# Performance work log

Measured on AMD Instinct MI355X. Metric: run time of the kernel, lower is better.

## Reference

```python
import jax, jax.numpy as jnp
import numpy as np

NUM_TASKS = 200_000
NUM_DATA = 100_000
E_DT = 1_000_000
E_TT = 1_000_000
N_DEV = 8
TASK_D, DATA_D, DEV_D, H = 12, 5, 12, 64


def _leaky(x):
    return jnp.where(x > 0, x, 0.01 * x)


def _layernorm(x, g, b, eps=1e-5):
    m = jnp.mean(x, axis=-1, keepdims=True)
    v = jnp.mean((x - m) ** 2, axis=-1, keepdims=True)
    return (x - m) * jax.lax.rsqrt(v + eps) * g + b


def _edge_conv(x, src, dst, W1, b1, W2, b2, n_nodes):
    # PyG EdgeConv: message = mlp(cat[x_i, x_j - x_i]), aggregated (add) at target i = dst
    xi = x[dst]                    # [E, d]
    xj = x[src]                    # [E, d]
    h = jnp.concatenate([xi, xj - xi], axis=-1)   # [E, 2d]
    h = _leaky(h @ W1 + b1)
    h = h @ W2 + b2
    return jax.ops.segment_sum(h, dst, num_segments=n_nodes)


def setup_inputs() -> dict:
    key = jax.random.key(0)
    ks = jax.random.split(key, 24)
    s = 0.05
    inp = {
        'data_x': jax.random.normal(ks[0], (NUM_DATA, DATA_D), jnp.float32),
        'tasks_x': jax.random.normal(ks[1], (NUM_TASKS, TASK_D), jnp.float32),
        'devices_x': jax.random.normal(ks[2], (N_DEV, DEV_D), jnp.float32),
        'time_x': jax.random.uniform(ks[3], (1, 1), jnp.float32) * 100000.0,
        'dt_src': jax.random.randint(ks[4], (E_DT,), 0, NUM_DATA, jnp.int32),
        'dt_dst': jax.random.randint(ks[5], (E_DT,), 0, NUM_TASKS, jnp.int32),
        'tt_src': jax.random.randint(ks[6], (E_TT,), 0, NUM_TASKS, jnp.int32),
        'tt_dst': jax.random.randint(ks[7], (E_TT,), 0, NUM_TASKS, jnp.int32),
        'counts': jax.random.randint(ks[8], (1,), 1, NUM_TASKS, jnp.int32),
        # GraphConv (bipartite): lin_rel on aggregated src msgs (with bias), lin_root on dst (no bias)
        'gc_W_rel': jax.random.normal(ks[9], (DATA_D, H), jnp.float32) * s,
        'gc_b_rel': jnp.zeros((H,), jnp.float32),
        'gc_W_root': jax.random.normal(ks[10], (TASK_D, H), jnp.float32) * s,
        'gc_ln_g': jnp.ones((H,), jnp.float32),
        'gc_ln_b': jnp.zeros((H,), jnp.float32),
        # EdgeConv dependants (edges as-is)
        'dep_W1': jax.random.normal(ks[11], (2 * H, H), jnp.float32) * s,
        'dep_b1': jnp.zeros((H,), jnp.float32),
        'dep_W2': jax.random.normal(ks[12], (H, H), jnp.float32) * s,
        'dep_b2': jnp.zeros((H,), jnp.float32),
        'dep_ln_g': jnp.ones((H,), jnp.float32),
        'dep_ln_b': jnp.zeros((H,), jnp.float32),
        # EdgeConv dependencies (edges flipped)
        'rev_W1': jax.random.normal(ks[13], (2 * H, H), jnp.float32) * s,
        'rev_b1': jnp.zeros((H,), jnp.float32),
        'rev_W2': jax.random.normal(ks[14], (H, H), jnp.float32) * s,
        'rev_b2': jnp.zeros((H,), jnp.float32),
        'rev_ln_g': jnp.ones((H,), jnp.float32),
        'rev_ln_b': jnp.zeros((H,), jnp.float32),
        # device layer: Linear(n_dev*dev_dim + 1 -> H)
        'dev_W': jax.random.normal(ks[15], (N_DEV * DEV_D + 1, H), jnp.float32) * s,
        'dev_b': jnp.zeros((H,), jnp.float32),
        # project down: Linear(2H -> H)
        'proj_W': jax.random.normal(ks[16], (2 * H, H), jnp.float32) * s,
        'proj_b': jnp.zeros((H,), jnp.float32),
    }
    return inp


def reference(data_x, tasks_x, devices_x, time_x, dt_src, dt_dst, tt_src, tt_dst, counts,
              gc_W_rel, gc_b_rel, gc_W_root, gc_ln_g, gc_ln_b,
              dep_W1, dep_b1, dep_W2, dep_b2, dep_ln_g, dep_ln_b,
              rev_W1, rev_b1, rev_W2, rev_b2, rev_ln_g, rev_ln_b,
              dev_W, dev_b, proj_W, proj_b):
    n_tasks = tasks_x.shape[0]
    # DataTaskGraphConv: scatter-add data features into tasks, then linear + root linear
    agg = jax.ops.segment_sum(data_x[dt_src], dt_dst, num_segments=n_tasks)  # [N_t, DATA_D]
    fused = agg @ gc_W_rel + gc_b_rel + tasks_x @ gc_W_root                  # [N_t, H]
    fused = _leaky(_layernorm(fused, gc_ln_g, gc_ln_b))
    # TaskTaskEdgeConv dependants (forward edges) and dependencies (flipped edges)
    dep = _edge_conv(fused, tt_src, tt_dst, dep_W1, dep_b1, dep_W2, dep_b2, n_tasks)
    dep = _leaky(_layernorm(dep, dep_ln_g, dep_ln_b))
    rev = _edge_conv(fused, tt_dst, tt_src, rev_W1, rev_b1, rev_W2, rev_b2, n_tasks)
    rev = _leaky(_layernorm(rev, rev_ln_g, rev_ln_b))
    # device branch
    dev = devices_x.reshape(-1)                      # [N_DEV*DEV_D]
    t = jax.lax.stop_gradient(time_x / 100000.0)[0]  # [1]
    dev = jnp.concatenate([dev, t], axis=-1)
    dev = _leaky(dev @ dev_W + dev_b)                # [H]
    # task fusion
    tf = jnp.concatenate([dep, rev], axis=-1)        # [N_t, 2H]
    tf = _leaky(tf @ proj_W + proj_b)                # [N_t, H]
    candidate = tf[0]                                # [H]
    c0 = jnp.maximum(counts[0], 1).astype(tf.dtype)
    global_state = jnp.sum(tf, axis=0) / c0          # [H]
    return jnp.concatenate([global_state, candidate, dev], axis=-1)  # [3H]
```

## Files before the change

### kernel.cpp

```cpp
#include <hip/hip_runtime.h>

#define DEVFN static __device__ __forceinline__

typedef __attribute__((ext_vector_type(8))) short short8;
typedef __attribute__((ext_vector_type(4))) float f32x4;

#define NB_SCAN 256
#define NB3 64
#define BUCKET 120
#define MAXBUK 2048

DEVFN float leaky(float x) { return x > 0.f ? x : 0.01f * x; }

DEVFN float wsum(float v) {
#pragma unroll
    for (int o = 32; o > 0; o >>= 1) v += __shfl_xor(v, o, 64);
    return v;
}

DEVFN unsigned short f2bf(float f) {
    unsigned u = __float_as_uint(f);
    unsigned r = (u + 0x7FFFu + ((u >> 16) & 1u)) >> 16;
    return (unsigned short)r;
}
DEVFN float bf2f(unsigned short h) { return __uint_as_float(((unsigned)h) << 16); }

__global__ void k_bhist(const int* __restrict__ tt_src, const int* __restrict__ tt_dst,
                        const int* __restrict__ dt_dst,
                        int* __restrict__ cnt_d, int* __restrict__ cnt_s, int* __restrict__ cnt_t,
                        int n_tt, int n_dt, int nbuk) {
    __shared__ int h[2 * MAXBUK];
    int blk = blockIdx.x, y = blockIdx.y;
    for (int k = threadIdx.x; k < nbuk; k += 256) {
        h[k] = 0;
        if (y == 0) h[MAXBUK + k] = 0;
    }
    __syncthreads();
    int n = (y == 0) ? n_tt : n_dt;
    int chunk = (n + NB3 - 1) / NB3;
    int e0 = blk * chunk;
    int e1 = e0 + chunk < n ? e0 + chunk : n;
    if (y == 0) {
        for (int i = e0 + threadIdx.x; i < e1; i += 256) {
            unsigned d = (unsigned)tt_dst[i], s = (unsigned)tt_src[i];
            atomicAdd(&h[d / BUCKET], 1);
            atomicAdd(&h[MAXBUK + s / BUCKET], 1);
        }
    } else {
        for (int i = e0 + threadIdx.x; i < e1; i += 256) {
            unsigned d = (unsigned)dt_dst[i];
            atomicAdd(&h[d / BUCKET], 1);
        }
    }
    __syncthreads();
    for (int k = threadIdx.x; k < nbuk; k += 256) {
        if (y == 0) {
            cnt_d[k * NB3 + blk] = h[k];
            cnt_s[k * NB3 + blk] = h[MAXBUK + k];
        } else {
            cnt_t[k * NB3 + blk] = h[k];
        }
    }
}

__global__ void k_scanA(const int* __restrict__ d0, const int* __restrict__ d1,
                        const int* __restrict__ d2, int* __restrict__ bsum, int n) {
    const int* deg = blockIdx.y == 0 ? d0 : (blockIdx.y == 1 ? d1 : d2);
    int chunk = (n + NB_SCAN - 1) / NB_SCAN;
    int base = blockIdx.x * chunk;
    int end = base + chunk;
    if (end > n) end = n;
    int s = 0;
    for (int i = base + threadIdx.x; i < end; i += 256) s += deg[i];
    int lane = threadIdx.x & 63, wid = threadIdx.x >> 6;
#pragma unroll
    for (int o = 32; o > 0; o >>= 1) s += __shfl_xor(s, o, 64);
    __shared__ int w[4];
    if (lane == 0) w[wid] = s;
    __syncthreads();
    if (threadIdx.x == 0) bsum[blockIdx.y * NB_SCAN + blockIdx.x] = w[0] + w[1] + w[2] + w[3];
}

__global__ void k_scanC(const int* __restrict__ d0, const int* __restrict__ d1,
                        const int* __restrict__ d2, const int* __restrict__ bsum,
                        int* __restrict__ o0, int* __restrict__ o1, int* __restrict__ o2,
                        int n) {
    const int* deg = blockIdx.y == 0 ? d0 : (blockIdx.y == 1 ? d1 : d2);
    int* off = blockIdx.y == 0 ? o0 : (blockIdx.y == 1 ? o1 : o2);
    __shared__ int bl[NB_SCAN];
    int t = threadIdx.x;
    int bv = bsum[blockIdx.y * NB_SCAN + t];
    bl[t] = bv;
    __syncthreads();
    for (int o = 1; o < NB_SCAN; o <<= 1) {
        int u = (t >= o) ? bl[t - o] : 0;
        __syncthreads();
        bl[t] += u;
        __syncthreads();
    }
    int blockpref = (blockIdx.x > 0) ? bl[blockIdx.x - 1] : 0;
    __syncthreads();

    int chunk = (n + NB_SCAN - 1) / NB_SCAN;
    int base = blockIdx.x * chunk;
    int end = base + chunk;
    if (end > n) end = n;
    int sub = (chunk + 255) >> 8;
    int s0 = base + t * sub;
    int s1 = s0 + sub;
    if (s0 > end) s0 = end;
    if (s1 > end) s1 = end;
    int s = 0;
    for (int i = s0; i < s1; ++i) s += deg[i];
    __shared__ int lds[256];
    lds[t] = s;
    __syncthreads();
    for (int o = 1; o < 256; o <<= 1) {
        int u = (t >= o) ? lds[t - o] : 0;
        __syncthreads();
        lds[t] += u;
        __syncthreads();
    }
    int ex = blockpref + lds[t] - s;
    for (int i = s0; i < s1; ++i) {
        off[i] = ex;
        ex += deg[i];
    }
}

__global__ void k_bdump(const int* __restrict__ tt_src, const int* __restrict__ tt_dst,
                        const int* __restrict__ dt_src, const int* __restrict__ dt_dst,
                        const int* __restrict__ base_d, const int* __restrict__ base_s,
                        const int* __restrict__ base_t,
                        unsigned* __restrict__ packed_d, unsigned* __restrict__ packed_s,
                        unsigned* __restrict__ packed_t,
                        int n_tt, int n_dt, int nbuk) {
    __shared__ int cur[2 * MAXBUK];
    int blk = blockIdx.x, y = blockIdx.y;
    for (int k = threadIdx.x; k < nbuk; k += 256) {
        if (y == 0) {
            cur[k] = base_d[k * NB3 + blk];
            cur[MAXBUK + k] = base_s[k * NB3 + blk];
        } else {
            cur[k] = base_t[k * NB3 + blk];
        }
    }
    __syncthreads();
    int n = (y == 0) ? n_tt : n_dt;
    int chunk = (n + NB3 - 1) / NB3;
    int e0 = blk * chunk;
    int e1 = e0 + chunk < n ? e0 + chunk : n;
    if (y == 0) {
        for (int i = e0 + threadIdx.x; i < e1; i += 256) {
            unsigned s = (unsigned)tt_src[i], d = (unsigned)tt_dst[i];
            unsigned bd = d / BUCKET, bs = s / BUCKET;
            int pd = atomicAdd(&cur[bd], 1);
            packed_d[pd] = ((d - bd * BUCKET) << 22) | s;
            int ps = atomicAdd(&cur[MAXBUK + bs], 1);
            packed_s[ps] = ((s - bs * BUCKET) << 22) | d;
        }
    } else {
        for (int i = e0 + threadIdx.x; i < e1; i += 256) {
            unsigned s = (unsigned)dt_src[i], d = (unsigned)dt_dst[i];
            unsigned bd = d / BUCKET;
            int pt = atomicAdd(&cur[bd], 1);
            packed_t[pt] = ((d - bd * BUCKET) << 22) | s;
        }
    }
}

__global__ void __launch_bounds__(256) k_bcsr(
    const unsigned* __restrict__ packed_d, const unsigned* __restrict__ packed_s,
    const int* __restrict__ base_d, const int* __restrict__ base_s,
    unsigned* __restrict__ other_d, unsigned* __restrict__ other_s,
    int* __restrict__ off_d, int* __restrict__ off_s,
    int* __restrict__ deg_d, int* __restrict__ deg_s,
    int n_tt, int n_tasks, int nbuk) {
    int y = blockIdx.y;
    const unsigned* packed = y ? packed_s : packed_d;
    const int* bases = y ? base_s : base_d;
    unsigned* other = y ? other_s : other_d;
    int* offo = y ? off_s : off_d;
    int* dego = y ? deg_s : deg_d;
    __shared__ int cnt[128];
    __shared__ int sc[128];
    __shared__ int cur[128];
    int tid = threadIdx.x;
    int b = blockIdx.x;
    int r0 = b * BUCKET;
    int rcount = n_tasks - r0 < BUCKET ? n_tasks - r0 : BUCKET;
    int a0 = bases[b * NB3];
    int a1 = (b + 1 < nbuk) ? bases[(b + 1) * NB3] : n_tt;
    if (tid < 128) cnt[tid] = 0;
    __syncthreads();
    for (int e = a0 + tid; e < a1; e += 256) atomicAdd(&cnt[packed[e] >> 22], 1);
    __syncthreads();
    if (tid < 128) sc[tid] = cnt[tid];
    __syncthreads();
    for (int o = 1; o < 128; o <<= 1) {
        int v = (tid >= o && tid < 128) ? sc[tid - o] : 0;
        __syncthreads();
        if (tid < 128) sc[tid] += v;
        __syncthreads();
    }
    if (tid < 128) {
        int ex = sc[tid] - cnt[tid];
        cur[tid] = ex;
        if (tid < rcount) {
            offo[r0 + tid] = a0 + ex;
            dego[r0 + tid] = cnt[tid];
        }
    }
    if (b == nbuk - 1 && tid == 0) offo[n_tasks] = n_tt;
    __syncthreads();
    for (int e = a0 + tid; e < a1; e += 256) {
        unsigned p = packed[e];
        int dl = p >> 22;
        int pos = atomicAdd(&cur[dl], 1);
        other[(size_t)a0 + pos] = p & 0x3FFFFF;
    }
}

__global__ void k_bagg(const float* __restrict__ data_x, const unsigned* __restrict__ packed_t,
                       const int* __restrict__ base_t, float* __restrict__ agg,
                       int n_dt, int n_tasks, int nbuk) {
    __shared__ float aggL[BUCKET * 5];
    int b = blockIdx.x;
    int r0 = b * BUCKET;
    int rcount = n_tasks - r0 < BUCKET ? n_tasks - r0 : BUCKET;
    for (int k = threadIdx.x; k < BUCKET * 5; k += 256) aggL[k] = 0.f;
    __syncthreads();
    int a0 = base_t[b * NB3];
    int a1 = (b + 1 < nbuk) ? base_t[(b + 1) * NB3] : n_dt;
    for (int e = a0 + threadIdx.x; e < a1; e += 256) {
        unsigned p = packed_t[e];
        int s = p & 0x3FFFFF;
        int dl = p >> 22;
        const float* xp = data_x + (size_t)s * 5;
#pragma unroll
        for (int c = 0; c < 5; ++c) atomicAdd(&aggL[dl * 5 + c], xp[c]);
    }
    __syncthreads();
    for (int k = threadIdx.x; k < rcount * 5; k += 256) agg[(size_t)r0 * 5 + k] = aggL[k];
}

__global__ void k_fused(const float* __restrict__ agg, const float* __restrict__ tasks_x,
                        const float* __restrict__ Wrel, const float* __restrict__ brel,
                        const float* __restrict__ Wroot,
                        const float* __restrict__ g, const float* __restrict__ b,
                        unsigned short* __restrict__ xh, int n_rows) {
    int lane = threadIdx.x & 63;
    int wave = (blockIdx.x * blockDim.x + threadIdx.x) >> 6;
    int nwaves = (gridDim.x * blockDim.x) >> 6;
    float wrel[5], wroot[12];
#pragma unroll
    for (int k = 0; k < 5; ++k) wrel[k] = Wrel[k * 64 + lane];
#pragma unroll
    for (int k = 0; k < 12; ++k) wroot[k] = Wroot[k * 64 + lane];
    float bj = brel[lane], gj = g[lane], bbj = b[lane];
    for (int r = wave; r < n_rows; r += nwaves) {
        float f = bj;
#pragma unroll
        for (int k = 0; k < 5; ++k) f = fmaf(agg[(size_t)r * 5 + k], wrel[k], f);
#pragma unroll
        for (int k = 0; k < 12; ++k) f = fmaf(tasks_x[(size_t)r * 12 + k], wroot[k], f);
        float m = wsum(f) * 0.015625f;
        float d = f - m;
        float v = wsum(d * d) * 0.015625f;
        float y = fmaf(d * rsqrtf(v + 1e-5f), gj, bbj);
        xh[(size_t)r * 64 + lane] = f2bf(leaky(y));
    }
}

__global__ void k_prepw(const float* __restrict__ W1d, const float* __restrict__ W2d,
                        const float* __restrict__ W1r, const float* __restrict__ W2r,
                        const float* __restrict__ PW, unsigned short* __restrict__ wf) {
    int lane = threadIdx.x;
    int r16 = lane & 15, g = lane >> 4;
    for (int c = 0; c < 2; ++c) {
        const float* W1 = c ? W1r : W1d;
        const float* W2 = c ? W2r : W2d;
        unsigned short* out = wf + (size_t)c * 48 * 512;
        for (int kk = 0; kk < 2; ++kk)
            for (int nt = 0; nt < 4; ++nt)
                for (int j = 0; j < 8; ++j) {
                    int k = kk * 32 + g * 8 + j, col = nt * 16 + r16;
                    int fr = (kk * 4 + nt) * 2;
                    float vc = W1[k * 64 + col] - W1[(64 + k) * 64 + col];
                    unsigned short hi = f2bf(vc);
                    out[(size_t)fr * 512 + lane * 8 + j] = hi;
                    out[(size_t)(fr + 1) * 512 + lane * 8 + j] = f2bf(vc - bf2f(hi));
                    float vt = W1[(64 + k) * 64 + col];
                    hi = f2bf(vt);
                    out[(size_t)(16 + fr) * 512 + lane * 8 + j] = hi;
                    out[(size_t)(16 + fr + 1) * 512 + lane * 8 + j] = f2bf(vt - bf2f(hi));
                    float v2 = W2[k * 64 + col];
                    hi = f2bf(v2);
                    out[(size_t)(32 + fr) * 512 + lane * 8 + j] = hi;
                    out[(size_t)(32 + fr + 1) * 512 + lane * 8 + j] = f2bf(v2 - bf2f(hi));
                }
    }
    unsigned short* out = wf + (size_t)96 * 512;
    for (int kk = 0; kk < 4; ++kk)
        for (int nt = 0; nt < 4; ++nt)
            for (int j = 0; j < 8; ++j) {
                int k = kk * 32 + g * 8 + j, col = nt * 16 + r16;
                int fr = (kk * 4 + nt) * 2;
                float v = PW[k * 64 + col];
                unsigned short hi = f2bf(v);
                out[(size_t)fr * 512 + lane * 8 + j] = hi;
                out[(size_t)(fr + 1) * 512 + lane * 8 + j] = f2bf(v - bf2f(hi));
            }
}

__global__ void __launch_bounds__(256, 2) k_ct(
    const unsigned short* __restrict__ xh, const unsigned short* __restrict__ wfall,
    const float* __restrict__ b1d, const float* __restrict__ b1r,
    unsigned short* __restrict__ Hd, unsigned short* __restrict__ Hr,
    unsigned short* __restrict__ Tbd, unsigned short* __restrict__ Tbr,
    int n_rows, int n_tiles) {
    int y = blockIdx.y;
    const unsigned short* wf = wfall + (size_t)y * 48 * 512;
    const float* b1 = y ? b1r : b1d;
    unsigned short* Cb = y ? Hr : Hd;
    unsigned short* Tb = y ? Tbr : Tbd;
    int lane = threadIdx.x & 63;
    int r16 = lane & 15, g = lane >> 4;
    int wave = (blockIdx.x * blockDim.x + threadIdx.x) >> 6;
    int nwaves = (gridDim.x * blockDim.x) >> 6;
    short8 cw[2][4][2], tw[2][4][2];
#pragma unroll
    for (int kk = 0; kk < 2; ++kk)
#pragma unroll
        for (int nt = 0; nt < 4; ++nt)
#pragma unroll
            for (int hl = 0; hl < 2; ++hl) {
                int fr = (kk * 4 + nt) * 2 + hl;
                cw[kk][nt][hl] = *(const short8*)(wf + (size_t)fr * 512 + lane * 8);
                tw[kk][nt][hl] = *(const short8*)(wf + (size_t)(16 + fr) * 512 + lane * 8);
            }
    float b1v[4];
#pragma unroll
    for (int nt = 0; nt < 4; ++nt) b1v[nt] = b1[nt * 16 + r16];
    for (int t = wave; t < n_tiles; t += nwaves) {
        int r0 = t * 16;
        int ra = r0 + r16;
        ra = ra < n_rows ? ra : n_rows - 1;
        short8 af[2];
        af[0] = *(const short8*)(xh + (size_t)ra * 64 + g * 8);
        af[1] = *(const short8*)(xh + (size_t)ra * 64 + 32 + g * 8);
        f32x4 accC[4], accT[4];
#pragma unroll
        for (int nt = 0; nt < 4; ++nt) {
            accC[nt] = (f32x4){b1v[nt], b1v[nt], b1v[nt], b1v[nt]};
            accT[nt] = (f32x4){0.f, 0.f, 0.f, 0.f};
        }
#pragma unroll
        for (int kk = 0; kk < 2; ++kk)
#pragma unroll
            for (int nt = 0; nt < 4; ++nt) {
                accC[nt] = __builtin_amdgcn_mfma_f32_16x16x32_bf16(af[kk], cw[kk][nt][0], accC[nt], 0, 0, 0);
                accC[nt] = __builtin_amdgcn_mfma_f32_16x16x32_bf16(af[kk], cw[kk][nt][1], accC[nt], 0, 0, 0);
                accT[nt] = __builtin_amdgcn_mfma_f32_16x16x32_bf16(af[kk], tw[kk][nt][0], accT[nt], 0, 0, 0);
                accT[nt] = __builtin_amdgcn_mfma_f32_16x16x32_bf16(af[kk], tw[kk][nt][1], accT[nt], 0, 0, 0);
            }
#pragma unroll
        for (int nt = 0; nt < 4; ++nt)
#pragma unroll
            for (int q = 0; q < 4; ++q) {
                int row = r0 + g * 4 + q;
                if (row < n_rows) {
                    Cb[(size_t)row * 64 + nt * 16 + r16] = f2bf(accC[nt][q]);
                    Tb[(size_t)row * 64 + nt * 16 + r16] = f2bf(accT[nt][q]);
                }
            }
    }
}

__global__ void k_edge(unsigned short* __restrict__ Hd, unsigned short* __restrict__ Hr,
                       const unsigned short* __restrict__ Tbd, const unsigned short* __restrict__ Tbr,
                       const int* __restrict__ off_d, const int* __restrict__ off_s,
                       const unsigned* __restrict__ other_d, const unsigned* __restrict__ other_s,
                       int n_tasks) {
    int lane = threadIdx.x & 63;
    int wave = (blockIdx.x * blockDim.x + threadIdx.x) >> 6;
    int nwaves = (gridDim.x * blockDim.x) >> 6;
    for (int i = wave; i < n_tasks; i += nwaves) {
        int pd = off_d[i], d1 = off_d[i + 1];
        int ps = off_s[i], s1 = off_s[i + 1];
        float cvd = bf2f(Hd[(size_t)i * 64 + lane]);
        float cvr = bf2f(Hr[(size_t)i * 64 + lane]);
        float accd = 0.f, accr = 0.f;
        while (pd + 2 <= d1 && ps + 2 <= s1) {
            unsigned jd0 = other_d[pd], jd1 = other_d[pd + 1];
            unsigned js0 = other_s[ps], js1 = other_s[ps + 1];
            float td0 = bf2f(Tbd[(size_t)jd0 * 64 + lane]);
            float td1 = bf2f(Tbd[(size_t)jd1 * 64 + lane]);
            float tr0 = bf2f(Tbr[(size_t)js0 * 64 + lane]);
            float tr1 = bf2f(Tbr[(size_t)js1 * 64 + lane]);
            accd += leaky(cvd + td0);
            accd += leaky(cvd + td1);
            accr += leaky(cvr + tr0);
            accr += leaky(cvr + tr1);
            pd += 2;
            ps += 2;
        }
        for (; pd + 4 <= d1; pd += 4) {
            float t0 = bf2f(Tbd[(size_t)other_d[pd] * 64 + lane]);
            float t1 = bf2f(Tbd[(size_t)other_d[pd + 1] * 64 + lane]);
            float t2 = bf2f(Tbd[(size_t)other_d[pd + 2] * 64 + lane]);
            float t3 = bf2f(Tbd[(size_t)other_d[pd + 3] * 64 + lane]);
            accd += leaky(cvd + t0);
            accd += leaky(cvd + t1);
            accd += leaky(cvd + t2);
            accd += leaky(cvd + t3);
        }
        for (; pd < d1; ++pd) accd += leaky(cvd + bf2f(Tbd[(size_t)other_d[pd] * 64 + lane]));
        for (; ps + 4 <= s1; ps += 4) {
            float t0 = bf2f(Tbr[(size_t)other_s[ps] * 64 + lane]);
            float t1 = bf2f(Tbr[(size_t)other_s[ps + 1] * 64 + lane]);
            float t2 = bf2f(Tbr[(size_t)other_s[ps + 2] * 64 + lane]);
            float t3 = bf2f(Tbr[(size_t)other_s[ps + 3] * 64 + lane]);
            accr += leaky(cvr + t0);
            accr += leaky(cvr + t1);
            accr += leaky(cvr + t2);
            accr += leaky(cvr + t3);
        }
        for (; ps < s1; ++ps) accr += leaky(cvr + bf2f(Tbr[(size_t)other_s[ps] * 64 + lane]));
        Hd[(size_t)i * 64 + lane] = f2bf(accd);
        Hr[(size_t)i * 64 + lane] = f2bf(accr);
    }
}

__global__ void __launch_bounds__(256, 2) k_post(
    unsigned short* __restrict__ Hd, unsigned short* __restrict__ Hr,
    const unsigned short* __restrict__ wfall,
    const float* __restrict__ b2d, const float* __restrict__ b2r,
    const int* __restrict__ deg_d, const int* __restrict__ deg_s,
    int n_rows, int n_tiles) {
    int y = blockIdx.y;
    unsigned short* H = y ? Hr : Hd;
    const unsigned short* wf = wfall + (size_t)(y ? 48 + 32 : 32) * 512;
    const float* b2 = y ? b2r : b2d;
    const int* deg = y ? deg_s : deg_d;
    int lane = threadIdx.x & 63;
    int r16 = lane & 15, g = lane >> 4;
    int wave = (blockIdx.x * blockDim.x + threadIdx.x) >> 6;
    int nwaves = (gridDim.x * blockDim.x) >> 6;
    short8 w2[2][4][2];
#pragma unroll
    for (int kk = 0; kk < 2; ++kk)
#pragma unroll
        for (int nt = 0; nt < 4; ++nt)
#pragma unroll
            for (int hl = 0; hl < 2; ++hl)
                w2[kk][nt][hl] =
                    *(const short8*)(wf + (size_t)((kk * 4 + nt) * 2 + hl) * 512 + lane * 8);
    float b2v[4];
#pragma unroll
    for (int nt = 0; nt < 4; ++nt) b2v[nt] = b2[nt * 16 + r16];
    for (int t = wave; t < n_tiles; t += nwaves) {
        int r0 = t * 16;
        int ra = r0 + r16;
        ra = ra < n_rows ? ra : n_rows - 1;
        short8 af[2];
        af[0] = *(const short8*)(H + (size_t)ra * 64 + g * 8);
        af[1] = *(const short8*)(H + (size_t)ra * 64 + 32 + g * 8);
        float degf[4];
#pragma unroll
        for (int q = 0; q < 4; ++q) {
            int r = r0 + g * 4 + q;
            r = r < n_rows ? r : n_rows - 1;
            degf[q] = (float)deg[r];
        }
        f32x4 acc[4];
#pragma unroll
        for (int nt = 0; nt < 4; ++nt)
#pragma unroll
            for (int q = 0; q < 4; ++q) acc[nt][q] = degf[q] * b2v[nt];
#pragma unroll
        for (int kk = 0; kk < 2; ++kk)
#pragma unroll
            for (int nt = 0; nt < 4; ++nt) {
                acc[nt] = __builtin_amdgcn_mfma_f32_16x16x32_bf16(af[kk], w2[kk][nt][0], acc[nt], 0, 0, 0);
                acc[nt] = __builtin_amdgcn_mfma_f32_16x16x32_bf16(af[kk], w2[kk][nt][1], acc[nt], 0, 0, 0);
            }
#pragma unroll
        for (int nt = 0; nt < 4; ++nt)
#pragma unroll
            for (int q = 0; q < 4; ++q) {
                int row = r0 + g * 4 + q;
                if (row < n_rows) H[(size_t)row * 64 + nt * 16 + r16] = f2bf(acc[nt][q]);
            }
    }
}

__global__ void __launch_bounds__(256, 2) k_finalize(
    const unsigned short* __restrict__ dep_raw, const unsigned short* __restrict__ rev_raw,
    const float* __restrict__ dg, const float* __restrict__ db,
    const float* __restrict__ rg, const float* __restrict__ rb,
    const unsigned short* __restrict__ pwf, const float* __restrict__ pb,
    float* __restrict__ out, float* __restrict__ gsum, int n_rows, int n_tiles) {
    __shared__ float red[4][64];
    int lane = threadIdx.x & 63;
    int wid = threadIdx.x >> 6;
    int r16 = lane & 15, g = lane >> 4;
    int wave = (blockIdx.x * blockDim.x + threadIdx.x) >> 6;
    int nwaves = (gridDim.x * blockDim.x) >> 6;

    short8 wf[4][4][2];
#pragma unroll
    for (int kk = 0; kk < 4; ++kk)
#pragma unroll
        for (int nt = 0; nt < 4; ++nt)
#pragma unroll
            for (int hl = 0; hl < 2; ++hl)
                wf[kk][nt][hl] =
                    *(const short8*)(pwf + (size_t)((kk * 4 + nt) * 2 + hl) * 512 + lane * 8);

    f32x4 gd0 = *(const f32x4*)(dg + g * 8), gd1 = *(const f32x4*)(dg + g * 8 + 4);
    f32x4 gd2 = *(const f32x4*)(dg + 32 + g * 8), gd3 = *(const f32x4*)(dg + 32 + g * 8 + 4);
    f32x4 bd0 = *(const f32x4*)(db + g * 8), bd1 = *(const f32x4*)(db + g * 8 + 4);
    f32x4 bd2 = *(const f32x4*)(db + 32 + g * 8), bd3 = *(const f32x4*)(db + 32 + g * 8 + 4);
    f32x4 gr0 = *(const f32x4*)(rg + g * 8), gr1 = *(const f32x4*)(rg + g * 8 + 4);
    f32x4 gr2 = *(const f32x4*)(rg + 32 + g * 8), gr3 = *(const f32x4*)(rg + 32 + g * 8 + 4);
    f32x4 br0 = *(const f32x4*)(rb + g * 8), br1 = *(const f32x4*)(rb + g * 8 + 4);
    f32x4 br2 = *(const f32x4*)(rb + 32 + g * 8), br3 = *(const f32x4*)(rb + 32 + g * 8 + 4);

    float b2v[4];
#pragma unroll
    for (int nt = 0; nt < 4; ++nt) b2v[nt] = pb[nt * 16 + r16];
    float gacc[4] = {0.f, 0.f, 0.f, 0.f};

    for (int t = wave; t < n_tiles; t += nwaves) {
        int r0 = t * 16;
        int ra = r0 + r16;
        ra = ra < n_rows ? ra : n_rows - 1;
        const unsigned short* dp = dep_raw + (size_t)ra * 64;
        const unsigned short* rp = rev_raw + (size_t)ra * 64;
        short8 hd0 = *(const short8*)(dp + g * 8);
        short8 hd1 = *(const short8*)(dp + 32 + g * 8);
        short8 hr0 = *(const short8*)(rp + g * 8);
        short8 hr1 = *(const short8*)(rp + 32 + g * 8);
        f32x4 xd0, xd1, xd2, xd3, xr0, xr1, xr2, xr3;
#pragma unroll
        for (int j = 0; j < 4; ++j) {
            xd0[j] = bf2f((unsigned short)hd0[j]);
            xd1[j] = bf2f((unsigned short)hd0[4 + j]);
            xd2[j] = bf2f((unsigned short)hd1[j]);
            xd3[j] = bf2f((unsigned short)hd1[4 + j]);
            xr0[j] = bf2f((unsigned short)hr0[j]);
            xr1[j] = bf2f((unsigned short)hr0[4 + j]);
            xr2[j] = bf2f((unsigned short)hr1[j]);
            xr3[j] = bf2f((unsigned short)hr1[4 + j]);
        }

        float sd = 0.f, qd = 0.f, sr = 0.f, qr = 0.f;
#pragma unroll
        for (int j = 0; j < 4; ++j) {
            sd += xd0[j] + xd1[j] + xd2[j] + xd3[j];
            qd = fmaf(xd0[j], xd0[j], qd); qd = fmaf(xd1[j], xd1[j], qd);
            qd = fmaf(xd2[j], xd2[j], qd); qd = fmaf(xd3[j], xd3[j], qd);
            sr += xr0[j] + xr1[j] + xr2[j] + xr3[j];
            qr = fmaf(xr0[j], xr0[j], qr); qr = fmaf(xr1[j], xr1[j], qr);
            qr = fmaf(xr2[j], xr2[j], qr); qr = fmaf(xr3[j], xr3[j], qr);
        }
#pragma unroll
        for (int o = 16; o <= 32; o <<= 1) {
            sd += __shfl_xor(sd, o, 64); qd += __shfl_xor(qd, o, 64);
            sr += __shfl_xor(sr, o, 64); qr += __shfl_xor(qr, o, 64);
        }
        float md = sd * 0.015625f;
        float rstd_d = rsqrtf(fmaf(qd, 0.015625f, -md * md) + 1e-5f);
        float mr = sr * 0.015625f;
        float rstd_r = rsqrtf(fmaf(qr, 0.015625f, -mr * mr) + 1e-5f);

        short8 af[4];
#pragma unroll
        for (int j = 0; j < 4; ++j) {
            af[0][j]     = (short)f2bf(leaky(fmaf((xd0[j] - md) * rstd_d, gd0[j], bd0[j])));
            af[0][4 + j] = (short)f2bf(leaky(fmaf((xd1[j] - md) * rstd_d, gd1[j], bd1[j])));
            af[1][j]     = (short)f2bf(leaky(fmaf((xd2[j] - md) * rstd_d, gd2[j], bd2[j])));
            af[1][4 + j] = (short)f2bf(leaky(fmaf((xd3[j] - md) * rstd_d, gd3[j], bd3[j])));
            af[2][j]     = (short)f2bf(leaky(fmaf((xr0[j] - mr) * rstd_r, gr0[j], br0[j])));
            af[2][4 + j] = (short)f2bf(leaky(fmaf((xr1[j] - mr) * rstd_r, gr1[j], br1[j])));
            af[3][j]     = (short)f2bf(leaky(fmaf((xr2[j] - mr) * rstd_r, gr2[j], br2[j])));
            af[3][4 + j] = (short)f2bf(leaky(fmaf((xr3[j] - mr) * rstd_r, gr3[j], br3[j])));
        }

        f32x4 acc[4];
#pragma unroll
        for (int nt = 0; nt < 4; ++nt) acc[nt] = (f32x4){b2v[nt], b2v[nt], b2v[nt], b2v[nt]};
#pragma unroll
        for (int kk = 0; kk < 4; ++kk)
#pragma unroll
            for (int nt = 0; nt < 4; ++nt) {
                acc[nt] = __builtin_amdgcn_mfma_f32_16x16x32_bf16(af[kk], wf[kk][nt][0], acc[nt], 0, 0, 0);
                acc[nt] = __builtin_amdgcn_mfma_f32_16x16x32_bf16(af[kk], wf[kk][nt][1], acc[nt], 0, 0, 0);
            }
#pragma unroll
        for (int nt = 0; nt < 4; ++nt)
#pragma unroll
            for (int q = 0; q < 4; ++q) {
                float tf = leaky(acc[nt][q]);
                int grow = r0 + g * 4 + q;
                if (grow < n_rows) gacc[nt] += tf;
                if (grow == 0) out[64 + nt * 16 + r16] = tf;
            }
    }
#pragma unroll
    for (int nt = 0; nt < 4; ++nt) {
        gacc[nt] += __shfl_xor(gacc[nt], 16, 64);
        gacc[nt] += __shfl_xor(gacc[nt], 32, 64);
    }
    if (g == 0) {
#pragma unroll
        for (int nt = 0; nt < 4; ++nt) red[wid][nt * 16 + r16] = gacc[nt];
    }
    __syncthreads();
    if (threadIdx.x < 64) {
        float ssum = red[0][threadIdx.x] + red[1][threadIdx.x] +
                     red[2][threadIdx.x] + red[3][threadIdx.x];
        atomicAdd(&gsum[threadIdx.x], ssum);
    }
}

__global__ void k_tail(const float* __restrict__ gsum, const int* __restrict__ counts,
                       const float* __restrict__ devx, const float* __restrict__ timex,
                       const float* __restrict__ dW, const float* __restrict__ dB,
                       float* __restrict__ out) {
    int j = threadIdx.x;
    if (j >= 64) return;
    int c = counts[0];
    if (c < 1) c = 1;
    out[j] = gsum[j] / (float)c;
    float t = timex[0] * 1e-5f;
    float acc = dB[j];
    for (int k = 0; k < 96; ++k) acc = fmaf(devx[k], dW[k * 64 + j], acc);
    acc = fmaf(t, dW[96 * 64 + j], acc);
    out[128 + j] = leaky(acc);
}

extern "C" void kernel_launch(void* const* d_in, const int* in_sizes, int n_in,
                              void* d_out, int out_size, void* d_ws, size_t ws_size,
                              hipStream_t stream) {
    const float* data_x    = (const float*)d_in[0];
    const float* tasks_x   = (const float*)d_in[1];
    const float* devices_x = (const float*)d_in[2];
    const float* time_x    = (const float*)d_in[3];
    const int*   dt_src    = (const int*)d_in[4];
    const int*   dt_dst    = (const int*)d_in[5];
    const int*   tt_src    = (const int*)d_in[6];
    const int*   tt_dst    = (const int*)d_in[7];
    const int*   counts    = (const int*)d_in[8];
    const float* gc_W_rel  = (const float*)d_in[9];
    const float* gc_b_rel  = (const float*)d_in[10];
    const float* gc_W_root = (const float*)d_in[11];
    const float* gc_ln_g   = (const float*)d_in[12];
    const float* gc_ln_b   = (const float*)d_in[13];
    const float* dep_W1    = (const float*)d_in[14];
    const float* dep_b1    = (const float*)d_in[15];
    const float* dep_W2    = (const float*)d_in[16];
    const float* dep_b2    = (const float*)d_in[17];
    const float* dep_ln_g  = (const float*)d_in[18];
    const float* dep_ln_b  = (const float*)d_in[19];
    const float* rev_W1    = (const float*)d_in[20];
    const float* rev_b1    = (const float*)d_in[21];
    const float* rev_W2    = (const float*)d_in[22];
    const float* rev_b2    = (const float*)d_in[23];
    const float* rev_ln_g  = (const float*)d_in[24];
    const float* rev_ln_b  = (const float*)d_in[25];
    const float* dev_W     = (const float*)d_in[26];
    const float* dev_b     = (const float*)d_in[27];
    const float* proj_W    = (const float*)d_in[28];
    const float* proj_b    = (const float*)d_in[29];

    int n_tasks = in_sizes[1] / 12;
    int n_dt = in_sizes[4];
    int n_tt = in_sizes[6];
    int n_tiles = (n_tasks + 15) / 16;
    int nbuk = (n_tasks + BUCKET - 1) / BUCKET;
    int nscan = nbuk * NB3;

    char* ws = (char*)d_ws;
    size_t off = 0;
    auto alloc = [&](size_t bytes) {
        char* p = ws + off;
        off += (bytes + 255) & ~(size_t)255;
        return p;
    };
    float* agg            = (float*)alloc((size_t)n_tasks * 5 * 4);
    unsigned short* xh    = (unsigned short*)alloc((size_t)n_tasks * 64 * 2);
    unsigned short* Hd    = (unsigned short*)alloc((size_t)n_tasks * 64 * 2);
    unsigned short* Hr    = (unsigned short*)alloc((size_t)n_tasks * 64 * 2);
    unsigned short* Tbd   = (unsigned short*)alloc((size_t)n_tasks * 64 * 2);
    unsigned short* Tbr   = (unsigned short*)alloc((size_t)n_tasks * 64 * 2);
    int* cnt_d            = (int*)alloc((size_t)nscan * 4);
    int* cnt_s            = (int*)alloc((size_t)nscan * 4);
    int* cnt_t            = (int*)alloc((size_t)nscan * 4);
    int* base_d           = (int*)alloc((size_t)nscan * 4);
    int* base_s           = (int*)alloc((size_t)nscan * 4);
    int* base_t           = (int*)alloc((size_t)nscan * 4);
    unsigned* packed_d    = (unsigned*)alloc((size_t)n_tt * 4);
    unsigned* packed_s    = (unsigned*)alloc((size_t)n_tt * 4);
    unsigned* packed_t    = (unsigned*)alloc((size_t)n_dt * 4);
    unsigned* other_d     = (unsigned*)alloc((size_t)n_tt * 4);
    unsigned* other_s     = (unsigned*)alloc((size_t)n_tt * 4);
    int* off_d            = (int*)alloc(((size_t)n_tasks + 1) * 4);
    int* off_s            = (int*)alloc(((size_t)n_tasks + 1) * 4);
    int* deg_d            = (int*)alloc((size_t)n_tasks * 4);
    int* deg_s            = (int*)alloc((size_t)n_tasks * 4);
    int* bsum             = (int*)alloc(3 * NB_SCAN * 4);
    float* gsum           = (float*)alloc(64 * 4);
    unsigned short* wfrag = (unsigned short*)alloc((size_t)128 * 512 * 2);

    hipMemsetAsync(gsum, 0, 64 * 4, stream);

    k_prepw<<<1, 64, 0, stream>>>(dep_W1, dep_W2, rev_W1, rev_W2, proj_W, wfrag);

    k_bhist<<<dim3(NB3, 2), 256, 0, stream>>>(tt_src, tt_dst, dt_dst,
                                              cnt_d, cnt_s, cnt_t, n_tt, n_dt, nbuk);
    k_scanA<<<dim3(NB_SCAN, 3), 256, 0, stream>>>(cnt_d, cnt_s, cnt_t, bsum, nscan);
    k_scanC<<<dim3(NB_SCAN, 3), 256, 0, stream>>>(cnt_d, cnt_s, cnt_t, bsum,
                                                  base_d, base_s, base_t, nscan);
    k_bdump<<<dim3(NB3, 2), 256, 0, stream>>>(tt_src, tt_dst, dt_src, dt_dst,
                                              base_d, base_s, base_t,
                                              packed_d, packed_s, packed_t, n_tt, n_dt, nbuk);
    k_bcsr<<<dim3(nbuk, 2), 256, 0, stream>>>(packed_d, packed_s, base_d, base_s,
                                              other_d, other_s, off_d, off_s,
                                              deg_d, deg_s, n_tt, n_tasks, nbuk);

    k_bagg<<<nbuk, 256, 0, stream>>>(data_x, packed_t, base_t, agg, n_dt, n_tasks, nbuk);
    k_fused<<<2048, 256, 0, stream>>>(agg, tasks_x, gc_W_rel, gc_b_rel, gc_W_root,
                                      gc_ln_g, gc_ln_b, xh, n_tasks);

    k_ct<<<dim3(2048, 2), 256, 0, stream>>>(xh, wfrag, dep_b1, rev_b1, Hd, Hr, Tbd, Tbr,
                                            n_tasks, n_tiles);
    k_edge<<<4096, 256, 0, stream>>>(Hd, Hr, Tbd, Tbr, off_d, off_s,
                                     other_d, other_s, n_tasks);
    k_post<<<dim3(2048, 2), 256, 0, stream>>>(Hd, Hr, wfrag, dep_b2, rev_b2,
                                              deg_d, deg_s, n_tasks, n_tiles);

    k_finalize<<<2048, 256, 0, stream>>>(Hd, Hr, dep_ln_g, dep_ln_b,
                                         rev_ln_g, rev_ln_b, wfrag + (size_t)96 * 512, proj_b,
                                         (float*)d_out, gsum, n_tasks, n_tiles);
    k_tail<<<1, 64, 0, stream>>>(gsum, counts, devices_x, time_x, dev_W, dev_b, (float*)d_out);
}
```

Baseline: 431.2 us.

## Fuse post-aggregation W2 GEMM, layernorm and projection into one kernel

```diff
diff --git a/kernel.cpp b/kernel.cpp
--- a/kernel.cpp
+++ b/kernel.cpp
@@ -277,40 +277,47 @@
                         const float* __restrict__ PW, unsigned short* __restrict__ wf) {
     int lane = threadIdx.x;
     int r16 = lane & 15, g = lane >> 4;
-    for (int c = 0; c < 2; ++c) {
+    int b = blockIdx.x;
+    if (b < 16) {
+        int c = b >> 3;
+        int tup = b & 7;
+        int kk = tup >> 2, nt = tup & 3;
         const float* W1 = c ? W1r : W1d;
         const float* W2 = c ? W2r : W2d;
         unsigned short* out = wf + (size_t)c * 48 * 512;
-        for (int kk = 0; kk < 2; ++kk)
-            for (int nt = 0; nt < 4; ++nt)
-                for (int j = 0; j < 8; ++j) {
-                    int k = kk * 32 + g * 8 + j, col = nt * 16 + r16;
-                    int fr = (kk * 4 + nt) * 2;
-                    float vc = W1[k * 64 + col] - W1[(64 + k) * 64 + col];
-                    unsigned short hi = f2bf(vc);
-                    out[(size_t)fr * 512 + lane * 8 + j] = hi;
-                    out[(size_t)(fr + 1) * 512 + lane * 8 + j] = f2bf(vc - bf2f(hi));
-                    float vt = W1[(64 + k) * 64 + col];
-                    hi = f2bf(vt);
-                    out[(size_t)(16 + fr) * 512 + lane * 8 + j] = hi;
-                    out[(size_t)(16 + fr + 1) * 512 + lane * 8 + j] = f2bf(vt - bf2f(hi));
-                    float v2 = W2[k * 64 + col];
-                    hi = f2bf(v2);
-                    out[(size_t)(32 + fr) * 512 + lane * 8 + j] = hi;
-                    out[(size_t)(32 + fr + 1) * 512 + lane * 8 + j] = f2bf(v2 - bf2f(hi));
-                }
-    }
-    unsigned short* out = wf + (size_t)96 * 512;
-    for (int kk = 0; kk < 4; ++kk)
-        for (int nt = 0; nt < 4; ++nt)
+        int fr = (kk * 4 + nt) * 2;
+#pragma unroll
+        for (int j = 0; j < 8; ++j) {
+            int k = kk * 32 + g * 8 + j, col = nt * 16 + r16;
+            float vc = W1[k * 64 + col] - W1[(64 + k) * 64 + col];
+            unsigned short hi = f2bf(vc);
+            out[(size_t)fr * 512 + lane * 8 + j] = hi;
+            out[(size_t)(fr + 1) * 512 + lane * 8 + j] = f2bf(vc - bf2f(hi));
+            float vt = W1[(64 + k) * 64 + col];
+            hi = f2bf(vt);
+            out[(size_t)(16 + fr) * 512 + lane * 8 + j] = hi;
+            out[(size_t)(16 + fr + 1) * 512 + lane * 8 + j] = f2bf(vt - bf2f(hi));
+            float v2 = W2[k * 64 + col];
+            hi = f2bf(v2);
+            out[(size_t)(32 + fr) * 512 + lane * 8 + j] = hi;
+            out[(size_t)(32 + fr + 1) * 512 + lane * 8 + j] = f2bf(v2 - bf2f(hi));
+        }
+    } else {
+        unsigned short* out = wf + (size_t)96 * 512;
+        int t0 = (b - 16) * 4;
+        for (int tt = t0; tt < t0 + 4; ++tt) {
+            int kk = tt >> 2, nt = tt & 3;
+            int fr = (kk * 4 + nt) * 2;
+#pragma unroll
             for (int j = 0; j < 8; ++j) {
                 int k = kk * 32 + g * 8 + j, col = nt * 16 + r16;
-                int fr = (kk * 4 + nt) * 2;
                 float v = PW[k * 64 + col];
                 unsigned short hi = f2bf(v);
                 out[(size_t)fr * 512 + lane * 8 + j] = hi;
                 out[(size_t)(fr + 1) * 512 + lane * 8 + j] = f2bf(v - bf2f(hi));
             }
+        }
+    }
 }
 
 __global__ void __launch_bounds__(256, 2) k_ct(
@@ -432,181 +439,167 @@
     }
 }
 
-__global__ void __launch_bounds__(256, 2) k_post(
-    unsigned short* __restrict__ Hd, unsigned short* __restrict__ Hr,
+__global__ void __launch_bounds__(256, 2) k_pf(
+    const unsigned short* __restrict__ Hd, const unsigned short* __restrict__ Hr,
     const unsigned short* __restrict__ wfall,
     const float* __restrict__ b2d, const float* __restrict__ b2r,
     const int* __restrict__ deg_d, const int* __restrict__ deg_s,
-    int n_rows, int n_tiles) {
-    int y = blockIdx.y;
-    unsigned short* H = y ? Hr : Hd;
-    const unsigned short* wf = wfall + (size_t)(y ? 48 + 32 : 32) * 512;
-    const float* b2 = y ? b2r : b2d;
-    const int* deg = y ? deg_s : deg_d;
-    int lane = threadIdx.x & 63;
-    int r16 = lane & 15, g = lane >> 4;
-    int wave = (blockIdx.x * blockDim.x + threadIdx.x) >> 6;
-    int nwaves = (gridDim.x * blockDim.x) >> 6;
-    short8 w2[2][4][2];
-#pragma unroll
-    for (int kk = 0; kk < 2; ++kk)
-#pragma unroll
-        for (int nt = 0; nt < 4; ++nt)
-#pragma unroll
-            for (int hl = 0; hl < 2; ++hl)
-                w2[kk][nt][hl] =
-                    *(const short8*)(wf + (size_t)((kk * 4 + nt) * 2 + hl) * 512 + lane * 8);
-    float b2v[4];
-#pragma unroll
-    for (int nt = 0; nt < 4; ++nt) b2v[nt] = b2[nt * 16 + r16];
-    for (int t = wave; t < n_tiles; t += nwaves) {
-        int r0 = t * 16;
-        int ra = r0 + r16;
-        ra = ra < n_rows ? ra : n_rows - 1;
-        short8 af[2];
-        af[0] = *(const short8*)(H + (size_t)ra * 64 + g * 8);
-        af[1] = *(const short8*)(H + (size_t)ra * 64 + 32 + g * 8);
-        float degf[4];
-#pragma unroll
-        for (int q = 0; q < 4; ++q) {
-            int r = r0 + g * 4 + q;
-            r = r < n_rows ? r : n_rows - 1;
-            degf[q] = (float)deg[r];
-        }
-        f32x4 acc[4];
-#pragma unroll
-        for (int nt = 0; nt < 4; ++nt)
-#pragma unroll
-            for (int q = 0; q < 4; ++q) acc[nt][q] = degf[q] * b2v[nt];
-#pragma unroll
-        for (int kk = 0; kk < 2; ++kk)
-#pragma unroll
-            for (int nt = 0; nt < 4; ++nt) {
-                acc[nt] = __builtin_amdgcn_mfma_f32_16x16x32_bf16(af[kk], w2[kk][nt][0], acc[nt], 0, 0, 0);
-                acc[nt] = __builtin_amdgcn_mfma_f32_16x16x32_bf16(af[kk], w2[kk][nt][1], acc[nt], 0, 0, 0);
-            }
-#pragma unroll
-        for (int nt = 0; nt < 4; ++nt)
-#pragma unroll
-            for (int q = 0; q < 4; ++q) {
-                int row = r0 + g * 4 + q;
-                if (row < n_rows) H[(size_t)row * 64 + nt * 16 + r16] = f2bf(acc[nt][q]);
-            }
-    }
-}
-
-__global__ void __launch_bounds__(256, 2) k_finalize(
-    const unsigned short* __restrict__ dep_raw, const unsigned short* __restrict__ rev_raw,
     const float* __restrict__ dg, const float* __restrict__ db,
     const float* __restrict__ rg, const float* __restrict__ rb,
-    const unsigned short* __restrict__ pwf, const float* __restrict__ pb,
+    const float* __restrict__ pb,
     float* __restrict__ out, float* __restrict__ gsum, int n_rows, int n_tiles) {
+    __shared__ unsigned short ldsT[4][16][136];
     __shared__ float red[4][64];
     int lane = threadIdx.x & 63;
-    int wid = threadIdx.x >> 6;
+    int w = threadIdx.x >> 6;
     int r16 = lane & 15, g = lane >> 4;
-    int wave = (blockIdx.x * blockDim.x + threadIdx.x) >> 6;
-    int nwaves = (gridDim.x * blockDim.x) >> 6;
-
-    short8 wf[4][4][2];
-#pragma unroll
-    for (int kk = 0; kk < 4; ++kk)
-#pragma unroll
-        for (int nt = 0; nt < 4; ++nt)
-#pragma unroll
-            for (int hl = 0; hl < 2; ++hl)
-                wf[kk][nt][hl] =
-                    *(const short8*)(pwf + (size_t)((kk * 4 + nt) * 2 + hl) * 512 + lane * 8);
-
-    f32x4 gd0 = *(const f32x4*)(dg + g * 8), gd1 = *(const f32x4*)(dg + g * 8 + 4);
-    f32x4 gd2 = *(const f32x4*)(dg + 32 + g * 8), gd3 = *(const f32x4*)(dg + 32 + g * 8 + 4);
-    f32x4 bd0 = *(const f32x4*)(db + g * 8), bd1 = *(const f32x4*)(db + g * 8 + 4);
-    f32x4 bd2 = *(const f32x4*)(db + 32 + g * 8), bd3 = *(const f32x4*)(db + 32 + g * 8 + 4);
-    f32x4 gr0 = *(const f32x4*)(rg + g * 8), gr1 = *(const f32x4*)(rg + g * 8 + 4);
-    f32x4 gr2 = *(const f32x4*)(rg + 32 + g * 8), gr3 = *(const f32x4*)(rg + 32 + g * 8 + 4);
-    f32x4 br0 = *(const f32x4*)(rb + g * 8), br1 = *(const f32x4*)(rb + g * 8 + 4);
-    f32x4 br2 = *(const f32x4*)(rb + 32 + g * 8), br3 = *(const f32x4*)(rb + 32 + g * 8 + 4);
-
-    float b2v[4];
-#pragma unroll
-    for (int nt = 0; nt < 4; ++nt) b2v[nt] = pb[nt * 16 + r16];
+
+    float gdv[4], bdv[4], grv[4], brv[4], b2dv[4], b2rv[4], pbv[4];
+#pragma unroll
+    for (int nt = 0; nt < 4; ++nt) {
+        int c = nt * 16 + r16;
+        gdv[nt] = dg[c]; bdv[nt] = db[c];
+        grv[nt] = rg[c]; brv[nt] = rb[c];
+        b2dv[nt] = b2d[c]; b2rv[nt] = b2r[c];
+        pbv[nt] = pb[c];
+    }
     float gacc[4] = {0.f, 0.f, 0.f, 0.f};
 
-    for (int t = wave; t < n_tiles; t += nwaves) {
-        int r0 = t * 16;
-        int ra = r0 + r16;
+    for (int t = blockIdx.x; t < n_tiles; t += gridDim.x) {
+        int R0 = t * 64 + w * 16;
+        int ra = R0 + r16;
         ra = ra < n_rows ? ra : n_rows - 1;
-        const unsigned short* dp = dep_raw + (size_t)ra * 64;
-        const unsigned short* rp = rev_raw + (size_t)ra * 64;
-        short8 hd0 = *(const short8*)(dp + g * 8);
-        short8 hd1 = *(const short8*)(dp + 32 + g * 8);
-        short8 hr0 = *(const short8*)(rp + g * 8);
-        short8 hr1 = *(const short8*)(rp + 32 + g * 8);
-        f32x4 xd0, xd1, xd2, xd3, xr0, xr1, xr2, xr3;
-#pragma unroll
-        for (int j = 0; j < 4; ++j) {
-            xd0[j] = bf2f((unsigned short)hd0[j]);
-            xd1[j] = bf2f((unsigned short)hd0[4 + j]);
-            xd2[j] = bf2f((unsigned short)hd1[j]);
-            xd3[j] = bf2f((unsigned short)hd1[4 + j]);
-            xr0[j] = bf2f((unsigned short)hr0[j]);
-            xr1[j] = bf2f((unsigned short)hr0[4 + j]);
-            xr2[j] = bf2f((unsigned short)hr1[j]);
-            xr3[j] = bf2f((unsigned short)hr1[4 + j]);
-        }
-
-        float sd = 0.f, qd = 0.f, sr = 0.f, qr = 0.f;
-#pragma unroll
-        for (int j = 0; j < 4; ++j) {
-            sd += xd0[j] + xd1[j] + xd2[j] + xd3[j];
-            qd = fmaf(xd0[j], xd0[j], qd); qd = fmaf(xd1[j], xd1[j], qd);
-            qd = fmaf(xd2[j], xd2[j], qd); qd = fmaf(xd3[j], xd3[j], qd);
-            sr += xr0[j] + xr1[j] + xr2[j] + xr3[j];
-            qr = fmaf(xr0[j], xr0[j], qr); qr = fmaf(xr1[j], xr1[j], qr);
-            qr = fmaf(xr2[j], xr2[j], qr); qr = fmaf(xr3[j], xr3[j], qr);
-        }
-#pragma unroll
-        for (int o = 16; o <= 32; o <<= 1) {
-            sd += __shfl_xor(sd, o, 64); qd += __shfl_xor(qd, o, 64);
-            sr += __shfl_xor(sr, o, 64); qr += __shfl_xor(qr, o, 64);
-        }
-        float md = sd * 0.015625f;
-        float rstd_d = rsqrtf(fmaf(qd, 0.015625f, -md * md) + 1e-5f);
-        float mr = sr * 0.015625f;
-        float rstd_r = rsqrtf(fmaf(qr, 0.015625f, -mr * mr) + 1e-5f);
-
-        short8 af[4];
-#pragma unroll
-        for (int j = 0; j < 4; ++j) {
-            af[0][j]     = (short)f2bf(leaky(fmaf((xd0[j] - md) * rstd_d, gd0[j], bd0[j])));
-            af[0][4 + j] = (short)f2bf(leaky(fmaf((xd1[j] - md) * rstd_d, gd1[j], bd1[j])));
-            af[1][j]     = (short)f2bf(leaky(fmaf((xd2[j] - md) * rstd_d, gd2[j], bd2[j])));
-            af[1][4 + j] = (short)f2bf(leaky(fmaf((xd3[j] - md) * rstd_d, gd3[j], bd3[j])));
-            af[2][j]     = (short)f2bf(leaky(fmaf((xr0[j] - mr) * rstd_r, gr0[j], br0[j])));
-            af[2][4 + j] = (short)f2bf(leaky(fmaf((xr1[j] - mr) * rstd_r, gr1[j], br1[j])));
-            af[3][j]     = (short)f2bf(leaky(fmaf((xr2[j] - mr) * rstd_r, gr2[j], br2[j])));
-            af[3][4 + j] = (short)f2bf(leaky(fmaf((xr3[j] - mr) * rstd_r, gr3[j], br3[j])));
-        }
-
-        f32x4 acc[4];
-#pragma unroll
-        for (int nt = 0; nt < 4; ++nt) acc[nt] = (f32x4){b2v[nt], b2v[nt], b2v[nt], b2v[nt]};
-#pragma unroll
-        for (int kk = 0; kk < 4; ++kk)
-#pragma unroll
-            for (int nt = 0; nt < 4; ++nt) {
-                acc[nt] = __builtin_amdgcn_mfma_f32_16x16x32_bf16(af[kk], wf[kk][nt][0], acc[nt], 0, 0, 0);
-                acc[nt] = __builtin_amdgcn_mfma_f32_16x16x32_bf16(af[kk], wf[kk][nt][1], acc[nt], 0, 0, 0);
-            }
-#pragma unroll
-        for (int nt = 0; nt < 4; ++nt)
+        {
+            short8 af[2];
+            af[0] = *(const short8*)(Hd + (size_t)ra * 64 + g * 8);
+            af[1] = *(const short8*)(Hd + (size_t)ra * 64 + 32 + g * 8);
+            f32x4 acc[4];
+            float degf[4];
 #pragma unroll
             for (int q = 0; q < 4; ++q) {
-                float tf = leaky(acc[nt][q]);
-                int grow = r0 + g * 4 + q;
-                if (grow < n_rows) gacc[nt] += tf;
-                if (grow == 0) out[64 + nt * 16 + r16] = tf;
-            }
+                int r = R0 + g * 4 + q;
+                r = r < n_rows ? r : n_rows - 1;
+                degf[q] = (float)deg_d[r];
+            }
+#pragma unroll
+            for (int nt = 0; nt < 4; ++nt)
+#pragma unroll
+                for (int q = 0; q < 4; ++q) acc[nt][q] = degf[q] * b2dv[nt];
+#pragma unroll
+            for (int kk = 0; kk < 2; ++kk)
+#pragma unroll
+                for (int nt = 0; nt < 4; ++nt) {
+                    int fr = 32 + (kk * 4 + nt) * 2;
+                    short8 w0 = *(const short8*)(wfall + (size_t)fr * 512 + lane * 8);
+                    short8 w1 = *(const short8*)(wfall + (size_t)(fr + 1) * 512 + lane * 8);
+                    acc[nt] = __builtin_amdgcn_mfma_f32_16x16x32_bf16(af[kk], w0, acc[nt], 0, 0, 0);
+                    acc[nt] = __builtin_amdgcn_mfma_f32_16x16x32_bf16(af[kk], w1, acc[nt], 0, 0, 0);
+                }
+            float s[4], qs[4];
+#pragma unroll
+            for (int q = 0; q < 4; ++q) {
+                s[q] = acc[0][q] + acc[1][q] + acc[2][q] + acc[3][q];
+                qs[q] = acc[0][q] * acc[0][q] + acc[1][q] * acc[1][q] +
+                        acc[2][q] * acc[2][q] + acc[3][q] * acc[3][q];
+            }
+#pragma unroll
+            for (int o = 1; o <= 8; o <<= 1)
+#pragma unroll
+                for (int q = 0; q < 4; ++q) {
+                    s[q] += __shfl_xor(s[q], o, 64);
+                    qs[q] += __shfl_xor(qs[q], o, 64);
+                }
+#pragma unroll
+            for (int q = 0; q < 4; ++q) {
+                float md = s[q] * 0.015625f;
+                float rstd = rsqrtf(fmaf(qs[q], 0.015625f, -md * md) + 1e-5f);
+#pragma unroll
+                for (int nt = 0; nt < 4; ++nt)
+                    ldsT[w][g * 4 + q][nt * 16 + r16] =
+                        f2bf(leaky(fmaf((acc[nt][q] - md) * rstd, gdv[nt], bdv[nt])));
+            }
+        }
+        {
+            short8 af[2];
+            af[0] = *(const short8*)(Hr + (size_t)ra * 64 + g * 8);
+            af[1] = *(const short8*)(Hr + (size_t)ra * 64 + 32 + g * 8);
+            f32x4 acc[4];
+            float degf[4];
+#pragma unroll
+            for (int q = 0; q < 4; ++q) {
+                int r = R0 + g * 4 + q;
+                r = r < n_rows ? r : n_rows - 1;
+                degf[q] = (float)deg_s[r];
+            }
+#pragma unroll
+            for (int nt = 0; nt < 4; ++nt)
+#pragma unroll
+                for (int q = 0; q < 4; ++q) acc[nt][q] = degf[q] * b2rv[nt];
+#pragma unroll
+            for (int kk = 0; kk < 2; ++kk)
+#pragma unroll
+                for (int nt = 0; nt < 4; ++nt) {
+                    int fr = 48 + 32 + (kk * 4 + nt) * 2;
+                    short8 w0 = *(const short8*)(wfall + (size_t)fr * 512 + lane * 8);
+                    short8 w1 = *(const short8*)(wfall + (size_t)(fr + 1) * 512 + lane * 8);
+                    acc[nt] = __builtin_amdgcn_mfma_f32_16x16x32_bf16(af[kk], w0, acc[nt], 0, 0, 0);
+                    acc[nt] = __builtin_amdgcn_mfma_f32_16x16x32_bf16(af[kk], w1, acc[nt], 0, 0, 0);
+                }
+            float s[4], qs[4];
+#pragma unroll
+            for (int q = 0; q < 4; ++q) {
+                s[q] = acc[0][q] + acc[1][q] + acc[2][q] + acc[3][q];
+                qs[q] = acc[0][q] * acc[0][q] + acc[1][q] * acc[1][q] +
+                        acc[2][q] * acc[2][q] + acc[3][q] * acc[3][q];
+            }
+#pragma unroll
+            for (int o = 1; o <= 8; o <<= 1)
+#pragma unroll
+                for (int q = 0; q < 4; ++q) {
+                    s[q] += __shfl_xor(s[q], o, 64);
+                    qs[q] += __shfl_xor(qs[q], o, 64);
+                }
+#pragma unroll
+            for (int q = 0; q < 4; ++q) {
+                float md = s[q] * 0.015625f;
+                float rstd = rsqrtf(fmaf(qs[q], 0.015625f, -md * md) + 1e-5f);
+#pragma unroll
+                for (int nt = 0; nt < 4; ++nt)
+                    ldsT[w][g * 4 + q][64 + nt * 16 + r16] =
+                        f2bf(leaky(fmaf((acc[nt][q] - md) * rstd, grv[nt], brv[nt])));
+            }
+        }
+        __syncthreads();
+        {
+            short8 a2[4];
+#pragma unroll
+            for (int kk = 0; kk < 4; ++kk)
+                a2[kk] = *(const short8*)&ldsT[w][r16][kk * 32 + g * 8];
+            f32x4 acc2[4];
+#pragma unroll
+            for (int nt = 0; nt < 4; ++nt)
+                acc2[nt] = (f32x4){pbv[nt], pbv[nt], pbv[nt], pbv[nt]};
+#pragma unroll
+            for (int kk = 0; kk < 4; ++kk)
+#pragma unroll
+                for (int nt = 0; nt < 4; ++nt) {
+                    int fr = 96 + (kk * 4 + nt) * 2;
+                    short8 w0 = *(const short8*)(wfall + (size_t)fr * 512 + lane * 8);
+                    short8 w1 = *(const short8*)(wfall + (size_t)(fr + 1) * 512 + lane * 8);
+                    acc2[nt] = __builtin_amdgcn_mfma_f32_16x16x32_bf16(a2[kk], w0, acc2[nt], 0, 0, 0);
+                    acc2[nt] = __builtin_amdgcn_mfma_f32_16x16x32_bf16(a2[kk], w1, acc2[nt], 0, 0, 0);
+                }
+#pragma unroll
+            for (int nt = 0; nt < 4; ++nt)
+#pragma unroll
+                for (int q = 0; q < 4; ++q) {
+                    float tf = leaky(acc2[nt][q]);
+                    int grow = t * 64 + w * 16 + g * 4 + q;
+                    if (grow < n_rows) gacc[nt] += tf;
+                    if (grow == 0) out[64 + nt * 16 + r16] = tf;
+                }
+        }
+        __syncthreads();
     }
 #pragma unroll
     for (int nt = 0; nt < 4; ++nt) {
@@ -615,7 +608,7 @@
     }
     if (g == 0) {
 #pragma unroll
-        for (int nt = 0; nt < 4; ++nt) red[wid][nt * 16 + r16] = gacc[nt];
+        for (int nt = 0; nt < 4; ++nt) red[w][nt * 16 + r16] = gacc[nt];
     }
     __syncthreads();
     if (threadIdx.x < 64) {
@@ -679,6 +672,7 @@
     int n_dt = in_sizes[4];
     int n_tt = in_sizes[6];
     int n_tiles = (n_tasks + 15) / 16;
+    int n_tiles64 = (n_tasks + 63) / 64;
     int nbuk = (n_tasks + BUCKET - 1) / BUCKET;
     int nscan = nbuk * NB3;
 
@@ -716,7 +710,7 @@
 
     hipMemsetAsync(gsum, 0, 64 * 4, stream);
 
-    k_prepw<<<1, 64, 0, stream>>>(dep_W1, dep_W2, rev_W1, rev_W2, proj_W, wfrag);
+    k_prepw<<<20, 64, 0, stream>>>(dep_W1, dep_W2, rev_W1, rev_W2, proj_W, wfrag);
 
     k_bhist<<<dim3(NB3, 2), 256, 0, stream>>>(tt_src, tt_dst, dt_dst,
                                               cnt_d, cnt_s, cnt_t, n_tt, n_dt, nbuk);
@@ -738,11 +732,9 @@
                                             n_tasks, n_tiles);
     k_edge<<<4096, 256, 0, stream>>>(Hd, Hr, Tbd, Tbr, off_d, off_s,
                                      other_d, other_s, n_tasks);
-    k_post<<<dim3(2048, 2), 256, 0, stream>>>(Hd, Hr, wfrag, dep_b2, rev_b2,
-                                              deg_d, deg_s, n_tasks, n_tiles);
-
-    k_finalize<<<2048, 256, 0, stream>>>(Hd, Hr, dep_ln_g, dep_ln_b,
-                                         rev_ln_g, rev_ln_b, wfrag + (size_t)96 * 512, proj_b,
-                                         (float*)d_out, gsum, n_tasks, n_tiles);
+
+    k_pf<<<n_tiles64, 256, 0, stream>>>(Hd, Hr, wfrag, dep_b2, rev_b2, deg_d, deg_s,
+                                        dep_ln_g, dep_ln_b, rev_ln_g, rev_ln_b, proj_b,
+                                        (float*)d_out, gsum, n_tasks, n_tiles64);
     k_tail<<<1, 64, 0, stream>>>(gsum, counts, devices_x, time_x, dev_W, dev_b, (float*)d_out);
 }
```

New measurement: 536.3 us. +24.4%, slower.
